# Kernel optimization log

Measured on AMD Instinct MI355X. Metric: run time of the kernel, lower is better.

The kernel has to match this reference:

```python
import jax, jax.numpy as jnp
import numpy as np

N = 4096
IN_F = 512
OUT_F = 512


def setup_inputs() -> dict:
    key = jax.random.key(0)
    k1, k2, k3, k4 = jax.random.split(key, 4)
    x = jax.random.normal(k1, (N, IN_F), dtype=jnp.float32)
    adj = jax.random.uniform(k2, (N, N), dtype=jnp.float32)
    # linear params (torch nn.Linear default init: U(-1/sqrt(fan_in), 1/sqrt(fan_in)))
    bound = 1.0 / np.sqrt(IN_F)
    W = jax.random.uniform(k3, (OUT_F, IN_F), minval=-bound, maxval=bound, dtype=jnp.float32)
    b = jax.random.uniform(k4, (OUT_F,), minval=-bound, maxval=bound, dtype=jnp.float32)
    return {"x": x, "adj": adj, "W": W, "b": b}


def reference(x, adj, W, b):
    # adj_hat = adj + I
    adj_hat = adj + jnp.eye(adj.shape[0], dtype=adj.dtype)
    # deg is diagonal with 1/sqrt(rowsum); deg @ adj @ deg == d[:,None] * adj * d[None,:]
    d = 1.0 / jnp.sqrt(adj_hat.sum(axis=1))  # [N]
    norm_adj = d[:, None] * adj_hat * d[None, :]  # [N, N]
    h = norm_adj @ x  # [N, in_features]
    return h @ W.T + b  # [N, out_features]
```

## Files before the change

kernel.cpp:

```cpp
#include <hip/hip_runtime.h>
#include <cstdint>

#define NN 4096
#define FF 512

typedef short bf16x8 __attribute__((ext_vector_type(8)));
typedef float f32x4 __attribute__((ext_vector_type(4)));
typedef float f32x16 __attribute__((ext_vector_type(16)));

__device__ __forceinline__ uint16_t f2bf(float f) {
    uint32_t u = __builtin_bit_cast(uint32_t, f);
    u += 0x7FFFu + ((u >> 16) & 1u);
    return (uint16_t)(u >> 16);
}
__device__ __forceinline__ float bf2f(uint16_t h) {
    uint32_t u = (uint32_t)h << 16;
    return __builtin_bit_cast(float, u);
}

__global__ __launch_bounds__(256) void k_prep(const float* __restrict__ adj,
                                              float* __restrict__ d,
                                              uint16_t* __restrict__ Abf) {
    const int row  = blockIdx.x * 4 + (threadIdx.x >> 6);
    const int lane = threadIdx.x & 63;
    const float4* p = (const float4*)(adj + (size_t)row * NN);
    float4 v[16];
    float s = 0.f;
#pragma unroll
    for (int i = 0; i < 16; ++i) {
        v[i] = p[lane + i * 64];
        s += (v[i].x + v[i].y) + (v[i].z + v[i].w);
    }
#pragma unroll
    for (int off = 1; off < 64; off <<= 1) s += __shfl_xor(s, off);
    const float di = rsqrtf(s + 1.0f);
    if (lane == 0) d[row] = di;
    uint16_t* outp = Abf + (size_t)row * NN;
#pragma unroll
    for (int i = 0; i < 16; ++i) {
        const int cb = (lane + i * 64) * 4;
        float a0 = v[i].x, a1 = v[i].y, a2 = v[i].z, a3 = v[i].w;
        if (cb + 0 == row) a0 += 1.0f;
        if (cb + 1 == row) a1 += 1.0f;
        if (cb + 2 == row) a2 += 1.0f;
        if (cb + 3 == row) a3 += 1.0f;
        ushort4 o;
        o.x = f2bf(a0); o.y = f2bf(a1); o.z = f2bf(a2); o.w = f2bf(a3);
        *(ushort4*)(outp + cb) = o;
    }
}

__global__ __launch_bounds__(256) void k_xc(const float* __restrict__ x,
                                            uint16_t* __restrict__ xbf) {
    const size_t t4 = (size_t)blockIdx.x * 256 + threadIdx.x;
    float4 v = *(const float4*)(x + t4 * 4);
    ushort4 o;
    o.x = f2bf(v.x); o.y = f2bf(v.y); o.z = f2bf(v.z); o.w = f2bf(v.w);
    *(ushort4*)(xbf + t4 * 4) = o;
}

__global__ __launch_bounds__(256) void k_wc(const float* __restrict__ W,
                                            uint16_t* __restrict__ Wbf) {
    const size_t t4 = (size_t)blockIdx.x * 256 + threadIdx.x;
    float4 v = *(const float4*)(W + t4 * 4);
    ushort4 o;
    o.x = f2bf(v.x); o.y = f2bf(v.y); o.z = f2bf(v.z); o.w = f2bf(v.w);
    *(ushort4*)(Wbf + t4 * 4) = o;
}

__global__ __launch_bounds__(256) void k_zt(const float* __restrict__ z32,
                                            const float* __restrict__ d,
                                            uint16_t* __restrict__ zdT) {
    __shared__ uint16_t t[64][72];
    const int k0 = blockIdx.x * 64;
    const int n0 = blockIdx.y * 64;
    const int tid = threadIdx.x;
    const int r   = tid >> 4;
    const int c4  = tid & 15;
#pragma unroll
    for (int pass = 0; pass < 4; ++pass) {
        const int row = pass * 16 + r;
        float4 v = *(const float4*)(z32 + (size_t)(k0 + row) * FF + n0 + c4 * 4);
        const float dk = d[k0 + row];
        t[c4 * 4 + 0][row] = f2bf(v.x * dk);
        t[c4 * 4 + 1][row] = f2bf(v.y * dk);
        t[c4 * 4 + 2][row] = f2bf(v.z * dk);
        t[c4 * 4 + 3][row] = f2bf(v.w * dk);
    }
    __syncthreads();
#pragma unroll
    for (int pass = 0; pass < 2; ++pass) {
        const int cid = pass * 256 + tid;
        const int n  = cid >> 3;
        const int ch = cid & 7;
        *(uint4*)(zdT + (size_t)(n0 + n) * NN + k0 + ch * 8) = *(const uint4*)&t[n][ch * 8];
    }
}

template <int BM, int BN, int K>
__global__ __launch_bounds__(256, 4) void k_mm(const uint16_t* __restrict__ A,
                                               const uint16_t* __restrict__ Bt,
                                               float* __restrict__ outp) {
    constexpr int NTC   = FF / BN;
    constexpr int NT    = K / 64;
    constexpr int MFR   = BM / 32;
    constexpr int NFR   = BN / 32;
    constexpr int LPT_A = BM / 32;
    constexpr int LPT_B = BN / 32;

    __shared__ uint16_t As[BM * 64];
    __shared__ uint16_t Bs[BN * 64];

    const int id   = blockIdx.x;
    const int mt   = id / NTC;
    const int nt   = id % NTC;
    const int m0 = mt * BM;
    const int n0 = nt * BN;

    const int tid  = threadIdx.x;
    const int w    = tid >> 6;
    const int lane = tid & 63;
    const int wm = w >> 1, wn = w & 1;

    f32x4 acc[MFR][NFR] = {};

    for (int t = 0; t < NT; ++t) {
        const int ktb = t * 64;
#pragma unroll
        for (int i = 0; i < LPT_A; ++i) {
            const int boff = i * 4096 + tid * 16;
            const int row  = boff >> 7;
            const int q    = (boff >> 4) & 7;
            const int c    = q ^ (row & 7);
            const uint16_t* src = A + (size_t)(m0 + row) * K + ktb + c * 8;
            __builtin_amdgcn_global_load_lds(
                (const __attribute__((address_space(1))) void*)src,
                (__attribute__((address_space(3))) void*)&As[boff >> 1],
                16, 0, 0);
        }
#pragma unroll
        for (int i = 0; i < LPT_B; ++i) {
            const int boff = i * 4096 + tid * 16;
            const int row  = boff >> 7;
            const int q    = (boff >> 4) & 7;
            const int c    = q ^ (row & 7);
            const uint16_t* src = Bt + (size_t)(n0 + row) * K + ktb + c * 8;
            __builtin_amdgcn_global_load_lds(
                (const __attribute__((address_space(1))) void*)src,
                (__attribute__((address_space(3))) void*)&Bs[boff >> 1],
                16, 0, 0);
        }
        __syncthreads();
#pragma unroll
        for (int kk = 0; kk < 2; ++kk) {
            const int cl = kk * 4 + (lane >> 4);
            bf16x8 af[MFR], bfr[NFR];
#pragma unroll
            for (int mf = 0; mf < MFR; ++mf) {
                const int r = wm * (MFR * 16) + mf * 16 + (lane & 15);
                af[mf] = *(const bf16x8*)&As[r * 64 + ((cl ^ (r & 7)) << 3)];
            }
#pragma unroll
            for (int nf = 0; nf < NFR; ++nf) {
                const int r = wn * (NFR * 16) + nf * 16 + (lane & 15);
                bfr[nf] = *(const bf16x8*)&Bs[r * 64 + ((cl ^ (r & 7)) << 3)];
            }
#pragma unroll
            for (int mf = 0; mf < MFR; ++mf)
#pragma unroll
                for (int nf = 0; nf < NFR; ++nf)
                    acc[mf][nf] = __builtin_amdgcn_mfma_f32_16x16x32_bf16(
                        af[mf], bfr[nf], acc[mf][nf], 0, 0, 0);
        }
        __syncthreads();
    }

    const int rbase = m0 + wm * (MFR * 16) + ((lane >> 4) << 2);
    const int cbase = n0 + wn * (NFR * 16) + (lane & 15);
#pragma unroll
    for (int mf = 0; mf < MFR; ++mf)
#pragma unroll
        for (int nf = 0; nf < NFR; ++nf) {
            const int col = cbase + nf * 16;
#pragma unroll
            for (int r = 0; r < 4; ++r) {
                const int row = rbase + mf * 16 + r;
                outp[(size_t)row * FF + col] = acc[mf][nf][r];
            }
        }
}

__global__ __launch_bounds__(256, 2) void k_mmx(const uint16_t* __restrict__ A,
                                                const uint16_t* __restrict__ Bt,
                                                uint16_t* __restrict__ parts) {
    constexpr int BM = 128, BN = 128, K = NN, SPLITK = 4;
    constexpr int NTC   = FF / BN;
    constexpr int KSLEN = K / SPLITK;
    constexpr int NT    = KSLEN / 64;
    constexpr int MTX   = (NN / BM) / 8;

    __shared__ uint16_t As[2][BM * 64];
    __shared__ uint16_t Bs[2][BN * 64];

    const int id   = blockIdx.x;
    const int xcd  = id & 7;
    const int slot = id >> 3;
    const int mt   = xcd * MTX + slot / (NTC * SPLITK);
    const int rem  = slot % (NTC * SPLITK);
    const int nt   = rem % NTC;
    const int ks   = rem / NTC;
    const int m0 = mt * BM;
    const int n0 = nt * BN;
    const int k0 = ks * KSLEN;

    const int tid  = threadIdx.x;
    const int w    = tid >> 6;
    const int lane = tid & 63;
    const int wm = w >> 1, wn = w & 1;

    f32x16 acc[2][2] = {};

    auto STAGE = [&](int t, int buf) {
        const int ktb = k0 + t * 64;
#pragma unroll
        for (int i = 0; i < 4; ++i) {
            const int boff = i * 4096 + tid * 16;
            const int row  = boff >> 7;
            const int q    = (boff >> 4) & 7;
            const int c    = q ^ (row & 7);
            const uint16_t* src = A + (size_t)(m0 + row) * K + ktb + c * 8;
            __builtin_amdgcn_global_load_lds(
                (const __attribute__((address_space(1))) void*)src,
                (__attribute__((address_space(3))) void*)&As[buf][boff >> 1],
                16, 0, 0);
        }
#pragma unroll
        for (int i = 0; i < 4; ++i) {
            const int boff = i * 4096 + tid * 16;
            const int row  = boff >> 7;
            const int q    = (boff >> 4) & 7;
            const int c    = q ^ (row & 7);
            const uint16_t* src = Bt + (size_t)(n0 + row) * K + ktb + c * 8;
            __builtin_amdgcn_global_load_lds(
                (const __attribute__((address_space(1))) void*)src,
                (__attribute__((address_space(3))) void*)&Bs[buf][boff >> 1],
                16, 0, 0);
        }
    };

    auto COMPUTE = [&](int buf) {
#pragma unroll
        for (int kk = 0; kk < 4; ++kk) {
            const int cl = kk * 2 + (lane >> 5);
            bf16x8 af[2], bfr[2];
#pragma unroll
            for (int mf = 0; mf < 2; ++mf) {
                const int r = wm * 64 + mf * 32 + (lane & 31);
                af[mf] = *(const bf16x8*)&As[buf][r * 64 + ((cl ^ (r & 7)) << 3)];
            }
#pragma unroll
            for (int nf = 0; nf < 2; ++nf) {
                const int r = wn * 64 + nf * 32 + (lane & 31);
                bfr[nf] = *(const bf16x8*)&Bs[buf][r * 64 + ((cl ^ (r & 7)) << 3)];
            }
#pragma unroll
            for (int mf = 0; mf < 2; ++mf)
#pragma unroll
                for (int nf = 0; nf < 2; ++nf)
                    acc[mf][nf] = __builtin_amdgcn_mfma_f32_32x32x16_bf16(
                        af[mf], bfr[nf], acc[mf][nf], 0, 0, 0);
        }
    };

    STAGE(0, 0);
    for (int t = 0; t < NT - 1; ++t) {
        STAGE(t + 1, (t + 1) & 1);
        asm volatile("s_waitcnt vmcnt(8)" ::: "memory");
        __builtin_amdgcn_s_barrier();
        COMPUTE(t & 1);
        __builtin_amdgcn_s_barrier();
    }
    asm volatile("s_waitcnt vmcnt(0)" ::: "memory");
    __builtin_amdgcn_s_barrier();
    COMPUTE((NT - 1) & 1);

    uint16_t* dst = parts + (size_t)ks * NN * FF;
    const int rb = m0 + wm * 64 + ((lane >> 5) << 2);
    const int cb = n0 + wn * 64 + (lane & 31);
#pragma unroll
    for (int mf = 0; mf < 2; ++mf)
#pragma unroll
        for (int nf = 0; nf < 2; ++nf) {
            const int gcol = cb + nf * 32;
#pragma unroll
            for (int r = 0; r < 16; ++r) {
                const int grow = rb + mf * 32 + (r & 3) + ((r >> 2) << 3);
                dst[(size_t)grow * FF + gcol] = f2bf(acc[mf][nf][r]);
            }
        }
}

__global__ __launch_bounds__(256) void k_red(const uint16_t* __restrict__ parts,
                                             const float* __restrict__ d,
                                             const float* __restrict__ b,
                                             float* __restrict__ out) {
    constexpr size_t STRIDE = (size_t)NN * FF;
    const size_t g   = (size_t)blockIdx.x * 256 + threadIdx.x;
    const int    row = (int)((g * 8) >> 9);
    const int    col = (int)((g * 8) & 511);
    float s[8] = {};
#pragma unroll
    for (int p = 0; p < 4; ++p) {
        ushort4 v0 = *(const ushort4*)(parts + p * STRIDE + g * 8);
        ushort4 v1 = *(const ushort4*)(parts + p * STRIDE + g * 8 + 4);
        s[0] += bf2f(v0.x); s[1] += bf2f(v0.y); s[2] += bf2f(v0.z); s[3] += bf2f(v0.w);
        s[4] += bf2f(v1.x); s[5] += bf2f(v1.y); s[6] += bf2f(v1.z); s[7] += bf2f(v1.w);
    }
    const float di = d[row];
    float4 o0, o1;
    o0.x = s[0] * di + b[col + 0];
    o0.y = s[1] * di + b[col + 1];
    o0.z = s[2] * di + b[col + 2];
    o0.w = s[3] * di + b[col + 3];
    o1.x = s[4] * di + b[col + 4];
    o1.y = s[5] * di + b[col + 5];
    o1.z = s[6] * di + b[col + 6];
    o1.w = s[7] * di + b[col + 7];
    *(float4*)(out + g * 8)     = o0;
    *(float4*)(out + g * 8 + 4) = o1;
}

extern "C" void kernel_launch(void* const* d_in, const int* in_sizes, int n_in,
                              void* d_out, int out_size, void* d_ws, size_t ws_size,
                              hipStream_t stream) {
    const float* x   = (const float*)d_in[0];
    const float* adj = (const float*)d_in[1];
    const float* W   = (const float*)d_in[2];
    const float* b   = (const float*)d_in[3];
    float* out = (float*)d_out;

    char* ws = (char*)d_ws;
    float*    d_    = (float*)ws;
    uint16_t* Abf   = (uint16_t*)(ws + 65536);
    uint16_t* zdT   = Abf + (size_t)NN * NN;
    uint16_t* xbf   = zdT + (size_t)FF * NN;
    uint16_t* Wbf   = xbf + (size_t)NN * FF;
    float*    z32   = (float*)(Wbf + (size_t)FF * FF);
    uint16_t* parts = (uint16_t*)(z32 + (size_t)NN * FF);

    k_wc<<<FF * FF / 1024, 256, 0, stream>>>(W, Wbf);
    k_xc<<<NN * FF / 1024, 256, 0, stream>>>(x, xbf);
    k_prep<<<NN / 4, 256, 0, stream>>>(adj, d_, Abf);
    k_mm<64, 64, FF><<<512, 256, 0, stream>>>(xbf, Wbf, z32);
    k_zt<<<dim3(NN / 64, FF / 64), 256, 0, stream>>>(z32, d_, zdT);
    k_mmx<<<512, 256, 0, stream>>>(Abf, zdT, parts);
    k_red<<<NN * FF / 2048, 256, 0, stream>>>(parts, d_, b, out);
}
```

Before: 68.73 us.

## Fuse d-scaling and transpose into x·Wᵀ GEMM epilogue, retile split-K adjacency GEMM

The x·Wᵀ GEMM now scales each row by d, converts to bf16 and writes the transposed zdT directly through an LDS tile. This removes the fp32 z32 intermediate and the separate transpose kernel. The large adj·z GEMM is retiled to 128x256 tiles with 512 threads, a 32-wide K step and split-K of 8 instead of 4. That doubles the bf16 partial-sum traffic read by the reduction kernel, in exchange for better operand reuse per block.

After: 70.20 us. +2.1%, slower.

```diff
diff --git a/kernel.cpp b/kernel.cpp
--- a/kernel.cpp
+++ b/kernel.cpp
@@ -13,8 +13,8 @@
     u += 0x7FFFu + ((u >> 16) & 1u);
     return (uint16_t)(u >> 16);
 }
-__device__ __forceinline__ float bf2f(uint16_t h) {
-    uint32_t u = (uint32_t)h << 16;
+__device__ __forceinline__ float bf2f(uint32_t h) {
+    uint32_t u = h << 16;
     return __builtin_bit_cast(float, u);
 }
 
@@ -68,52 +68,21 @@
     *(ushort4*)(Wbf + t4 * 4) = o;
 }
 
-__global__ __launch_bounds__(256) void k_zt(const float* __restrict__ z32,
-                                            const float* __restrict__ d,
-                                            uint16_t* __restrict__ zdT) {
-    __shared__ uint16_t t[64][72];
-    const int k0 = blockIdx.x * 64;
-    const int n0 = blockIdx.y * 64;
-    const int tid = threadIdx.x;
-    const int r   = tid >> 4;
-    const int c4  = tid & 15;
-#pragma unroll
-    for (int pass = 0; pass < 4; ++pass) {
-        const int row = pass * 16 + r;
-        float4 v = *(const float4*)(z32 + (size_t)(k0 + row) * FF + n0 + c4 * 4);
-        const float dk = d[k0 + row];
-        t[c4 * 4 + 0][row] = f2bf(v.x * dk);
-        t[c4 * 4 + 1][row] = f2bf(v.y * dk);
-        t[c4 * 4 + 2][row] = f2bf(v.z * dk);
-        t[c4 * 4 + 3][row] = f2bf(v.w * dk);
-    }
-    __syncthreads();
-#pragma unroll
-    for (int pass = 0; pass < 2; ++pass) {
-        const int cid = pass * 256 + tid;
-        const int n  = cid >> 3;
-        const int ch = cid & 7;
-        *(uint4*)(zdT + (size_t)(n0 + n) * NN + k0 + ch * 8) = *(const uint4*)&t[n][ch * 8];
-    }
-}
-
-template <int BM, int BN, int K>
-__global__ __launch_bounds__(256, 4) void k_mm(const uint16_t* __restrict__ A,
-                                               const uint16_t* __restrict__ Bt,
-                                               float* __restrict__ outp) {
-    constexpr int NTC   = FF / BN;
-    constexpr int NT    = K / 64;
-    constexpr int MFR   = BM / 32;
-    constexpr int NFR   = BN / 32;
-    constexpr int LPT_A = BM / 32;
-    constexpr int LPT_B = BN / 32;
+__global__ __launch_bounds__(256, 4) void k_mmz(const uint16_t* __restrict__ A,
+                                                const uint16_t* __restrict__ Bt,
+                                                const float* __restrict__ d,
+                                                uint16_t* __restrict__ zdT) {
+    constexpr int BM = 64, BN = 64, K = FF;
+    constexpr int NTC = FF / BN;
+    constexpr int NT  = K / 64;
 
     __shared__ uint16_t As[BM * 64];
     __shared__ uint16_t Bs[BN * 64];
-
-    const int id   = blockIdx.x;
-    const int mt   = id / NTC;
-    const int nt   = id % NTC;
+    __shared__ uint16_t tt[64][80];
+
+    const int id = blockIdx.x;
+    const int mt = id / NTC;
+    const int nt = id % NTC;
     const int m0 = mt * BM;
     const int n0 = nt * BN;
 
@@ -122,12 +91,12 @@
     const int lane = tid & 63;
     const int wm = w >> 1, wn = w & 1;
 
-    f32x4 acc[MFR][NFR] = {};
+    f32x4 acc[2][2] = {};
 
     for (int t = 0; t < NT; ++t) {
         const int ktb = t * 64;
 #pragma unroll
-        for (int i = 0; i < LPT_A; ++i) {
+        for (int i = 0; i < 2; ++i) {
             const int boff = i * 4096 + tid * 16;
             const int row  = boff >> 7;
             const int q    = (boff >> 4) & 7;
@@ -139,7 +108,7 @@
                 16, 0, 0);
         }
 #pragma unroll
-        for (int i = 0; i < LPT_B; ++i) {
+        for (int i = 0; i < 2; ++i) {
             const int boff = i * 4096 + tid * 16;
             const int row  = boff >> 7;
             const int q    = (boff >> 4) & 7;
@@ -154,61 +123,65 @@
 #pragma unroll
         for (int kk = 0; kk < 2; ++kk) {
             const int cl = kk * 4 + (lane >> 4);
-            bf16x8 af[MFR], bfr[NFR];
-#pragma unroll
-            for (int mf = 0; mf < MFR; ++mf) {
-                const int r = wm * (MFR * 16) + mf * 16 + (lane & 15);
+            bf16x8 af[2], bfr[2];
+#pragma unroll
+            for (int mf = 0; mf < 2; ++mf) {
+                const int r = wm * 32 + mf * 16 + (lane & 15);
                 af[mf] = *(const bf16x8*)&As[r * 64 + ((cl ^ (r & 7)) << 3)];
             }
 #pragma unroll
-            for (int nf = 0; nf < NFR; ++nf) {
-                const int r = wn * (NFR * 16) + nf * 16 + (lane & 15);
+            for (int nf = 0; nf < 2; ++nf) {
+                const int r = wn * 32 + nf * 16 + (lane & 15);
                 bfr[nf] = *(const bf16x8*)&Bs[r * 64 + ((cl ^ (r & 7)) << 3)];
             }
 #pragma unroll
-            for (int mf = 0; mf < MFR; ++mf)
-#pragma unroll
-                for (int nf = 0; nf < NFR; ++nf)
+            for (int mf = 0; mf < 2; ++mf)
+#pragma unroll
+                for (int nf = 0; nf < 2; ++nf)
                     acc[mf][nf] = __builtin_amdgcn_mfma_f32_16x16x32_bf16(
                         af[mf], bfr[nf], acc[mf][nf], 0, 0, 0);
         }
         __syncthreads();
     }
 
-    const int rbase = m0 + wm * (MFR * 16) + ((lane >> 4) << 2);
-    const int cbase = n0 + wn * (NFR * 16) + (lane & 15);
-#pragma unroll
-    for (int mf = 0; mf < MFR; ++mf)
-#pragma unroll
-        for (int nf = 0; nf < NFR; ++nf) {
-            const int col = cbase + nf * 16;
+    const int rb = wm * 32 + ((lane >> 4) << 2);
+    const int cb = wn * 32 + (lane & 15);
+#pragma unroll
+    for (int mf = 0; mf < 2; ++mf)
+#pragma unroll
+        for (int nf = 0; nf < 2; ++nf) {
+            const int col_l = cb + nf * 16;
 #pragma unroll
             for (int r = 0; r < 4; ++r) {
-                const int row = rbase + mf * 16 + r;
-                outp[(size_t)row * FF + col] = acc[mf][nf][r];
-            }
-        }
-}
-
-__global__ __launch_bounds__(256, 2) void k_mmx(const uint16_t* __restrict__ A,
+                const int row_l = rb + mf * 16 + r;
+                tt[col_l][row_l] = f2bf(acc[mf][nf][r] * d[m0 + row_l]);
+            }
+        }
+    __syncthreads();
+    const int n_l = tid >> 2;
+    const int ch  = tid & 3;
+    uint4* dst = (uint4*)(zdT + (size_t)(n0 + n_l) * NN + m0 + ch * 16);
+    dst[0] = *(const uint4*)&tt[n_l][ch * 16];
+    dst[1] = *(const uint4*)&tt[n_l][ch * 16 + 8];
+}
+
+__global__ __launch_bounds__(512, 2) void k_mmx(const uint16_t* __restrict__ A,
                                                 const uint16_t* __restrict__ Bt,
                                                 uint16_t* __restrict__ parts) {
-    constexpr int BM = 128, BN = 128, K = NN, SPLITK = 4;
-    constexpr int NTC   = FF / BN;
+    constexpr int BM = 128, BN = 256, K = NN, SPLITK = 8;
     constexpr int KSLEN = K / SPLITK;
-    constexpr int NT    = KSLEN / 64;
-    constexpr int MTX   = (NN / BM) / 8;
-
-    __shared__ uint16_t As[2][BM * 64];
-    __shared__ uint16_t Bs[2][BN * 64];
+    constexpr int NT    = KSLEN / 32;
+
+    __shared__ uint16_t As[2][BM * 32];
+    __shared__ uint16_t Bs[2][BN * 32];
 
     const int id   = blockIdx.x;
     const int xcd  = id & 7;
     const int slot = id >> 3;
-    const int mt   = xcd * MTX + slot / (NTC * SPLITK);
-    const int rem  = slot % (NTC * SPLITK);
-    const int nt   = rem % NTC;
-    const int ks   = rem / NTC;
+    const int mt   = xcd * 4 + (slot >> 4);
+    const int rem  = slot & 15;
+    const int ks   = rem >> 1;
+    const int nt   = rem & 1;
     const int m0 = mt * BM;
     const int n0 = nt * BN;
     const int k0 = ks * KSLEN;
@@ -216,18 +189,17 @@
     const int tid  = threadIdx.x;
     const int w    = tid >> 6;
     const int lane = tid & 63;
-    const int wm = w >> 1, wn = w & 1;
+    const int wm = w >> 2, wn = w & 3;
 
     f32x16 acc[2][2] = {};
 
     auto STAGE = [&](int t, int buf) {
-        const int ktb = k0 + t * 64;
-#pragma unroll
-        for (int i = 0; i < 4; ++i) {
-            const int boff = i * 4096 + tid * 16;
-            const int row  = boff >> 7;
-            const int q    = (boff >> 4) & 7;
-            const int c    = q ^ (row & 7);
+        const int ktb = k0 + t * 32;
+        {
+            const int boff = tid * 16;
+            const int row  = boff >> 6;
+            const int q    = (boff >> 4) & 3;
+            const int c    = q ^ (row & 3);
             const uint16_t* src = A + (size_t)(m0 + row) * K + ktb + c * 8;
             __builtin_amdgcn_global_load_lds(
                 (const __attribute__((address_space(1))) void*)src,
@@ -235,11 +207,11 @@
                 16, 0, 0);
         }
 #pragma unroll
-        for (int i = 0; i < 4; ++i) {
-            const int boff = i * 4096 + tid * 16;
-            const int row  = boff >> 7;
-            const int q    = (boff >> 4) & 7;
-            const int c    = q ^ (row & 7);
+        for (int i = 0; i < 2; ++i) {
+            const int boff = i * 8192 + tid * 16;
+            const int row  = boff >> 6;
+            const int q    = (boff >> 4) & 3;
+            const int c    = q ^ (row & 3);
             const uint16_t* src = Bt + (size_t)(n0 + row) * K + ktb + c * 8;
             __builtin_amdgcn_global_load_lds(
                 (const __attribute__((address_space(1))) void*)src,
@@ -250,18 +222,18 @@
 
     auto COMPUTE = [&](int buf) {
 #pragma unroll
-        for (int kk = 0; kk < 4; ++kk) {
+        for (int kk = 0; kk < 2; ++kk) {
             const int cl = kk * 2 + (lane >> 5);
             bf16x8 af[2], bfr[2];
 #pragma unroll
             for (int mf = 0; mf < 2; ++mf) {
                 const int r = wm * 64 + mf * 32 + (lane & 31);
-                af[mf] = *(const bf16x8*)&As[buf][r * 64 + ((cl ^ (r & 7)) << 3)];
+                af[mf] = *(const bf16x8*)&As[buf][r * 32 + ((cl ^ (r & 3)) << 3)];
             }
 #pragma unroll
             for (int nf = 0; nf < 2; ++nf) {
                 const int r = wn * 64 + nf * 32 + (lane & 31);
-                bfr[nf] = *(const bf16x8*)&Bs[buf][r * 64 + ((cl ^ (r & 7)) << 3)];
+                bfr[nf] = *(const bf16x8*)&Bs[buf][r * 32 + ((cl ^ (r & 3)) << 3)];
             }
 #pragma unroll
             for (int mf = 0; mf < 2; ++mf)
@@ -275,7 +247,7 @@
     STAGE(0, 0);
     for (int t = 0; t < NT - 1; ++t) {
         STAGE(t + 1, (t + 1) & 1);
-        asm volatile("s_waitcnt vmcnt(8)" ::: "memory");
+        asm volatile("s_waitcnt vmcnt(3)" ::: "memory");
         __builtin_amdgcn_s_barrier();
         COMPUTE(t & 1);
         __builtin_amdgcn_s_barrier();
@@ -310,7 +282,7 @@
     const int    col = (int)((g * 8) & 511);
     float s[8] = {};
 #pragma unroll
-    for (int p = 0; p < 4; ++p) {
+    for (int p = 0; p < 8; ++p) {
         ushort4 v0 = *(const ushort4*)(parts + p * STRIDE + g * 8);
         ushort4 v1 = *(const ushort4*)(parts + p * STRIDE + g * 8 + 4);
         s[0] += bf2f(v0.x); s[1] += bf2f(v0.y); s[2] += bf2f(v0.z); s[3] += bf2f(v0.w);
@@ -345,14 +317,12 @@
     uint16_t* zdT   = Abf + (size_t)NN * NN;
     uint16_t* xbf   = zdT + (size_t)FF * NN;
     uint16_t* Wbf   = xbf + (size_t)NN * FF;
-    float*    z32   = (float*)(Wbf + (size_t)FF * FF);
-    uint16_t* parts = (uint16_t*)(z32 + (size_t)NN * FF);
+    uint16_t* parts = Wbf + (size_t)FF * FF;
 
     k_wc<<<FF * FF / 1024, 256, 0, stream>>>(W, Wbf);
     k_xc<<<NN * FF / 1024, 256, 0, stream>>>(x, xbf);
     k_prep<<<NN / 4, 256, 0, stream>>>(adj, d_, Abf);
-    k_mm<64, 64, FF><<<512, 256, 0, stream>>>(xbf, Wbf, z32);
-    k_zt<<<dim3(NN / 64, FF / 64), 256, 0, stream>>>(z32, d_, zdT);
-    k_mmx<<<512, 256, 0, stream>>>(Abf, zdT, parts);
+    k_mmz<<<512, 256, 0, stream>>>(xbf, Wbf, d_, zdT);
+    k_mmx<<<512, 512, 0, stream>>>(Abf, zdT, parts);
     k_red<<<NN * FF / 2048, 256, 0, stream>>>(parts, d_, b, out);
 }
```
